# Performance work log

Measured on AMD Instinct MI355X. Metric: run time of the kernel, lower is better.

The kernel has to match this reference:

```python
import jax, jax.numpy as jnp
import numpy as np

GROUPS = 256   # B: number of index groups
SEQ = 512      # L: tokens per group (equal-length groups)
D_IN = 128
D_QK = 64
D_V = 128


def setup_inputs() -> dict:
    key = jax.random.key(0)
    ks = jax.random.split(key, 7)
    N = GROUPS * SEQ
    inputs = jax.random.normal(ks[0], (N, D_IN), dtype=jnp.float32)
    # sorted group ids: GROUPS groups of SEQ tokens each
    index = jnp.repeat(jnp.arange(GROUPS, dtype=jnp.int64), SEQ)
    s_in = 1.0 / np.sqrt(D_IN)
    Wq = jax.random.normal(ks[1], (D_IN, D_QK), dtype=jnp.float32) * s_in
    bq = jax.random.normal(ks[2], (D_QK,), dtype=jnp.float32) * 0.01
    Wk = jax.random.normal(ks[3], (D_IN, D_QK), dtype=jnp.float32) * s_in
    bk = jax.random.normal(ks[4], (D_QK,), dtype=jnp.float32) * 0.01
    Wv = jax.random.normal(ks[5], (D_IN, D_V), dtype=jnp.float32) * s_in
    bv = jax.random.normal(ks[6], (D_V,), dtype=jnp.float32) * 0.01
    return {"inputs": inputs, "index": index, "Wq": Wq, "bq": bq,
            "Wk": Wk, "bk": bk, "Wv": Wv, "bv": bv}


def reference(inputs, index, Wq, bq, Wk, bk, Wv, bv):
    # Linear projections on flat tokens [N, d]
    q = inputs @ Wq + bq          # [N, D_QK]
    k = inputs @ Wk + bk          # [N, D_QK]
    v = inputs @ Wv + bv          # [N, D_V]
    # unbatch: equal-length sorted groups -> [B, L, d]
    q = q.reshape(GROUPS, SEQ, D_QK)
    k = k.reshape(GROUPS, SEQ, D_QK)
    v = v.reshape(GROUPS, SEQ, D_V)
    # note the module's scale: sqrt(2 * d_qk)
    scale = 1.0 / np.sqrt(2.0 * D_QK).astype(np.float32)
    scores = jnp.einsum('bqd,bkd->bqk', q, k) * scale   # [B, L, L]
    attn = jax.nn.softmax(scores, axis=-1)
    out = jnp.einsum('bqk,bkd->bqd', attn, v)           # [B, L, D_V]
    return out.reshape(-1, D_V)                          # [N, D_V]
```

## Files before the change

kernel.cpp:

```cpp
#include <hip/hip_runtime.h>
#include <hip/hip_bf16.h>
#include <stdint.h>

#define GROUPS 256
#define SEQ    512
#define D_IN   128
#define D_QK   64
#define D_V    128
#define NTOK   (GROUPS * SEQ)

#define SL2E (0.08838834764831845f * 1.4426950408889634f)

typedef short bf8 __attribute__((ext_vector_type(8)));
typedef short bf4 __attribute__((ext_vector_type(4)));
typedef float f32x4 __attribute__((ext_vector_type(4)));

__device__ __forceinline__ short f2bf(float f) {
    __bf16 h = (__bf16)f;
    return __builtin_bit_cast(short, h);
}

__device__ __forceinline__ void gload_lds16(const void* g, void* l) {
    __builtin_amdgcn_global_load_lds(
        (const __attribute__((address_space(1))) unsigned int*)(uintptr_t)(g),
        (__attribute__((address_space(3))) unsigned int*)(uint32_t)(uintptr_t)(l),
        16, 0, 0);
}

__global__ __launch_bounds__(256) void prep_w(
    const float* __restrict__ Wq, const float* __restrict__ bq,
    const float* __restrict__ Wk, const float* __restrict__ bk,
    const float* __restrict__ Wv, const float* __restrict__ bv,
    short* __restrict__ Wt, float* __restrict__ bcat)
{
    const int t = blockIdx.x * 256 + threadIdx.x;
    const int r  = t >> 5;
    const int k0 = (t & 31) * 4;
    const float* W; int ld; int c; float sc;
    if (r < 64)       { W = Wq; ld = 64;  c = r;       sc = SL2E; }
    else if (r < 128) { W = Wk; ld = 64;  c = r - 64;  sc = 1.0f; }
    else              { W = Wv; ld = 128; c = r - 128; sc = 1.0f; }
    bf4 pk;
#pragma unroll
    for (int i = 0; i < 4; ++i) pk[i] = f2bf(W[(size_t)(k0 + i) * ld + c] * sc);
    const int phys = (k0 * 2) ^ ((r & 7) << 4);
    *reinterpret_cast<bf4*>((char*)Wt + r * 256 + phys) = pk;
    if (t < 256) {
        const float* b = (t < 64) ? bq : (t < 128 ? bk : bv);
        const int cb   = (t < 64) ? t  : (t < 128 ? t - 64 : t - 128);
        bcat[t] = b[cb] * (t < 64 ? SL2E : 1.0f);
    }
}

__global__ __launch_bounds__(256) void proj_kernel(
    const float* __restrict__ x, const short* __restrict__ Wt,
    const float* __restrict__ bcat,
    short* __restrict__ Q, short* __restrict__ K, short* __restrict__ Vt)
{
    __shared__ short wlds[16384];
    const int tid = threadIdx.x;
    const int wid = tid >> 6, lane = tid & 63, l15 = lane & 15, lg = lane >> 4;

#pragma unroll
    for (int i = 0; i < 8; ++i)
        gload_lds16((const char*)Wt + i * 4096 + tid * 16,
                    (char*)wlds + i * 4096 + tid * 16);

    const size_t tw = (size_t)blockIdx.x * 128 + wid * 32;
    const int g     = (int)(tw >> 9);
    const int tseg  = (int)(tw & 511);

    bf8 xf[2][4];
#pragma unroll
    for (int m = 0; m < 2; ++m) {
        const float* xr = x + (tw + m * 16 + l15) * D_IN;
#pragma unroll
        for (int kf = 0; kf < 4; ++kf) {
            const float4 a = *reinterpret_cast<const float4*>(xr + kf * 32 + lg * 8);
            const float4 b = *reinterpret_cast<const float4*>(xr + kf * 32 + lg * 8 + 4);
            bf8 v;
            v[0] = f2bf(a.x); v[1] = f2bf(a.y); v[2] = f2bf(a.z); v[3] = f2bf(a.w);
            v[4] = f2bf(b.x); v[5] = f2bf(b.y); v[6] = f2bf(b.z); v[7] = f2bf(b.w);
            xf[m][kf] = v;
        }
    }
    __syncthreads();

#pragma unroll
    for (int cf = 0; cf < 8; ++cf) {
        const int wrow = cf * 16 + l15;
        bf8 wf[4];
#pragma unroll
        for (int kf = 0; kf < 4; ++kf) {
            const int off = (kf * 64 + lg * 16) ^ ((wrow & 7) << 4);
            wf[kf] = *reinterpret_cast<const bf8*>((const char*)wlds + wrow * 256 + off);
        }
        const float4 bias4 = *reinterpret_cast<const float4*>(bcat + cf * 16 + lg * 4);
#pragma unroll
        for (int m = 0; m < 2; ++m) {
            f32x4 acc = (f32x4){0.f, 0.f, 0.f, 0.f};
#pragma unroll
            for (int kf = 0; kf < 4; ++kf)
                acc = __builtin_amdgcn_mfma_f32_16x16x32_bf16(wf[kf], xf[m][kf], acc, 0, 0, 0);
            bf4 pk;
            pk[0] = f2bf(acc[0] + bias4.x); pk[1] = f2bf(acc[1] + bias4.y);
            pk[2] = f2bf(acc[2] + bias4.z); pk[3] = f2bf(acc[3] + bias4.w);
            const size_t tok = tw + m * 16 + l15;
            if (cf < 4) {
                *reinterpret_cast<bf4*>((char*)Q + tok * 128 + cf * 32 + lg * 8) = pk;
            } else {
                const int lo = ((cf - 4) * 32 + lg * 8) ^ (((int)tok & 7) << 4);
                *reinterpret_cast<bf4*>((char*)K + tok * 128 + lo) = pk;
            }
        }
    }
    __syncthreads();

#pragma unroll
    for (int i = 0; i < 8; ++i)
        gload_lds16((const char*)Wt + 32768 + i * 4096 + tid * 16,
                    (char*)wlds + i * 4096 + tid * 16);
    __syncthreads();

#pragma unroll
    for (int cf = 8; cf < 16; ++cf) {
        const int lrow = (cf - 8) * 16 + l15;
        bf8 wf[4];
#pragma unroll
        for (int kf = 0; kf < 4; ++kf) {
            const int off = (kf * 64 + lg * 16) ^ ((lrow & 7) << 4);
            wf[kf] = *reinterpret_cast<const bf8*>((const char*)wlds + lrow * 256 + off);
        }
        const int d = (cf - 8) * 16 + l15;
        const float bias = bcat[cf * 16 + l15];
        const int sd = (d >> 1) & 3;
        char* vg = (char*)Vt + (size_t)g * 131072 + (size_t)d * 64;
#pragma unroll
        for (int m = 0; m < 2; ++m) {
            f32x4 acc = (f32x4){0.f, 0.f, 0.f, 0.f};
#pragma unroll
            for (int kf = 0; kf < 4; ++kf)
                acc = __builtin_amdgcn_mfma_f32_16x16x32_bf16(xf[m][kf], wf[kf], acc, 0, 0, 0);
            bf4 pk;
#pragma unroll
            for (int r = 0; r < 4; ++r) pk[r] = f2bf(acc[r] + bias);
            const int t0    = tseg + m * 16;
            const int inner = ((lg ^ sd) << 4) + ((t0 >> 4) & 1) * 8;
            *reinterpret_cast<bf4*>(vg + (size_t)(t0 >> 5) * 8192 + inner) = pk;
        }
    }
}

__global__ __launch_bounds__(256, 4) void attn_kernel(
    const short* __restrict__ Q, const short* __restrict__ K,
    const short* __restrict__ Vt, float* __restrict__ out)
{
    __shared__ short lds[2 * 6144];
    const int g = blockIdx.x, rb = blockIdx.y;
    const int tid = threadIdx.x, wid = tid >> 6, lane = tid & 63;
    const int l15 = lane & 15, lg = lane >> 4;
    const size_t gtok = (size_t)g * SEQ;
    const int row0 = rb * 128 + wid * 32;

    bf8 qf[2][2];
#pragma unroll
    for (int rf = 0; rf < 2; ++rf) {
        const short* qr = Q + (gtok + row0 + rf * 16 + l15) * 64 + lg * 8;
        qf[rf][0] = *reinterpret_cast<const bf8*>(qr);
        qf[rf][1] = *reinterpret_cast<const bf8*>(qr + 32);
    }

    const char* Kg = (const char*)(K + gtok * 64);
    const char* Vg = (const char*)Vt + (size_t)g * 131072;

    f32x4 o[2][8];
#pragma unroll
    for (int rf = 0; rf < 2; ++rf)
#pragma unroll
        for (int vt = 0; vt < 8; ++vt) o[rf][vt] = (f32x4){0.f, 0.f, 0.f, 0.f};
    f32x4 psv[2] = {(f32x4){0.f, 0.f, 0.f, 0.f}, (f32x4){0.f, 0.f, 0.f, 0.f}};
    const bf8 onesf = {0x3F80, 0x3F80, 0x3F80, 0x3F80, 0x3F80, 0x3F80, 0x3F80, 0x3F80};

    auto stage = [&](int kt, int b) {
        char* lbase = (char*)lds + b * 12288;
        int c = wid * 3;
#pragma unroll
        for (int i = 0; i < 3; ++i, ++c) {
            if (c < 4) {
                gload_lds16(Kg + (size_t)kt * 4096 + c * 1024 + lane * 16,
                            lbase + c * 1024 + lane * 16);
            } else {
                gload_lds16(Vg + (size_t)kt * 8192 + (c - 4) * 1024 + lane * 16,
                            lbase + c * 1024 + lane * 16);
            }
        }
    };

    auto compute = [&](int b) {
        const char* lb = (const char*)lds + b * 12288;
        __builtin_amdgcn_s_setprio(1);
        f32x4 st[2][2];
#pragma unroll
        for (int tf = 0; tf < 2; ++tf) {
            const int tok = tf * 16 + l15;
            const char* kb = lb + tok * 128;
            const int x7 = (tok & 7) << 4;
            const bf8 k0 = *reinterpret_cast<const bf8*>(kb + ((lg * 16) ^ x7));
            const bf8 k1 = *reinterpret_cast<const bf8*>(kb + ((64 + lg * 16) ^ x7));
#pragma unroll
            for (int rf = 0; rf < 2; ++rf) {
                f32x4 s = (f32x4){0.f, 0.f, 0.f, 0.f};
                s = __builtin_amdgcn_mfma_f32_16x16x32_bf16(k0, qf[rf][0], s, 0, 0, 0);
                s = __builtin_amdgcn_mfma_f32_16x16x32_bf16(k1, qf[rf][1], s, 0, 0, 0);
                st[tf][rf] = s;
            }
        }
        bf8 pa[2];
#pragma unroll
        for (int rf = 0; rf < 2; ++rf) {
            bf8 pv;
#pragma unroll
            for (int i = 0; i < 4; ++i) {
                pv[i]     = f2bf(__builtin_amdgcn_exp2f(st[0][rf][i]));
                pv[i + 4] = f2bf(__builtin_amdgcn_exp2f(st[1][rf][i]));
            }
            pa[rf] = pv;
            psv[rf] = __builtin_amdgcn_mfma_f32_16x16x32_bf16(pv, onesf, psv[rf], 0, 0, 0);
        }
        const char* vb = lb + 4096;
#pragma unroll
        for (int vt = 0; vt < 8; ++vt) {
            const int d = vt * 16 + l15;
            const char* vr = vb + d * 64;
            const bf8 v0 = *reinterpret_cast<const bf8*>(vr + ((lg * 16) ^ ((((d >> 1) & 3)) << 4)));
            o[0][vt] = __builtin_amdgcn_mfma_f32_16x16x32_bf16(pa[0], v0, o[0][vt], 0, 0, 0);
            o[1][vt] = __builtin_amdgcn_mfma_f32_16x16x32_bf16(pa[1], v0, o[1][vt], 0, 0, 0);
        }
        __builtin_amdgcn_s_setprio(0);
    };

    stage(0, 0);
    __syncthreads();
    for (int kt = 0; kt < 16; ++kt) {
        const int b = kt & 1;
        if (kt < 15) stage(kt + 1, b ^ 1);
        compute(b);
        __syncthreads();
    }

#pragma unroll
    for (int rf = 0; rf < 2; ++rf) {
        float linv[4];
#pragma unroll
        for (int r = 0; r < 4; ++r) linv[r] = 1.0f / psv[rf][r];
        float* op = out + (gtok + row0 + rf * 16) * D_V;
#pragma unroll
        for (int vt = 0; vt < 8; ++vt)
#pragma unroll
            for (int r = 0; r < 4; ++r)
                op[(size_t)(lg * 4 + r) * D_V + vt * 16 + l15] = o[rf][vt][r] * linv[r];
    }
}

extern "C" void kernel_launch(void* const* d_in, const int* in_sizes, int n_in,
                              void* d_out, int out_size, void* d_ws, size_t ws_size,
                              hipStream_t stream) {
    (void)in_sizes; (void)n_in; (void)ws_size; (void)out_size;
    const float* x  = (const float*)d_in[0];
    const float* Wq = (const float*)d_in[2];
    const float* bq = (const float*)d_in[3];
    const float* Wk = (const float*)d_in[4];
    const float* bk = (const float*)d_in[5];
    const float* Wv = (const float*)d_in[6];
    const float* bv = (const float*)d_in[7];
    float* out = (float*)d_out;

    short* Qw = (short*)d_ws;
    short* Kw = Qw + (size_t)NTOK * D_QK;
    short* Vt = Kw + (size_t)NTOK * D_QK;

    short* Wt   = (short*)out;
    float* bcat = (float*)((char*)out + 65536);

    prep_w<<<32, 256, 0, stream>>>(Wq, bq, Wk, bk, Wv, bv, Wt, bcat);
    proj_kernel<<<NTOK / 128, 256, 0, stream>>>(x, Wt, bcat, Qw, Kw, Vt);
    attn_kernel<<<dim3(GROUPS, 4), 256, 0, stream>>>(Qw, Kw, Vt, out);
}
```

Baseline: 67.96 us.

## Fuse QKV projection into attention kernel, one block per group

Merges the projection and attention kernels into one kernel that runs one 512-thread block per group. Q is projected once into registers, and K/V are recomputed per 32-token tile from x staged in LDS. This removes the Q/K/Vt workspace round-trip through global memory and one launch. In exchange, the grid drops from 1024 blocks to 256 blocks, each using about 108KB of LDS and many registers, which lowers occupancy and parallelism. Every K/V projection step now sits on the critical path, separated from the attention math by an added barrier.

```diff
diff --git a/kernel.cpp b/kernel.cpp
--- a/kernel.cpp
+++ b/kernel.cpp
@@ -5,8 +5,6 @@
 #define GROUPS 256
 #define SEQ    512
 #define D_IN   128
-#define D_QK   64
-#define D_V    128
 #define NTOK   (GROUPS * SEQ)
 
 #define SL2E (0.08838834764831845f * 1.4426950408889634f)
@@ -52,28 +50,27 @@
     }
 }
 
-__global__ __launch_bounds__(256) void proj_kernel(
+__global__ __launch_bounds__(512, 2) void fused_kernel(
     const float* __restrict__ x, const short* __restrict__ Wt,
-    const float* __restrict__ bcat,
-    short* __restrict__ Q, short* __restrict__ K, short* __restrict__ Vt)
+    const float* __restrict__ bcat, float* __restrict__ out)
 {
-    __shared__ short wlds[16384];
+    extern __shared__ char smem[];
     const int tid = threadIdx.x;
-    const int wid = tid >> 6, lane = tid & 63, l15 = lane & 15, lg = lane >> 4;
+    const int w = tid >> 6, lane = tid & 63, l15 = lane & 15, lg = lane >> 4;
+    const int g = blockIdx.x;
+    char* Wl  = smem;
+    char* xb0 = smem + 65536;
+    char* xb1 = smem + 81920;
+    char* kv  = smem + 98304;
 
 #pragma unroll
     for (int i = 0; i < 8; ++i)
-        gload_lds16((const char*)Wt + i * 4096 + tid * 16,
-                    (char*)wlds + i * 4096 + tid * 16);
-
-    const size_t tw = (size_t)blockIdx.x * 128 + wid * 32;
-    const int g     = (int)(tw >> 9);
-    const int tseg  = (int)(tw & 511);
-
-    bf8 xf[2][4];
-#pragma unroll
-    for (int m = 0; m < 2; ++m) {
-        const float* xr = x + (tw + m * 16 + l15) * D_IN;
+        gload_lds16((const char*)Wt + i * 8192 + tid * 16, Wl + i * 8192 + tid * 16);
+
+    bf8 xq[4][4];
+#pragma unroll
+    for (int rf = 0; rf < 4; ++rf) {
+        const float* xr = x + ((size_t)g * SEQ + w * 64 + rf * 16 + l15) * D_IN;
 #pragma unroll
         for (int kf = 0; kf < 4; ++kf) {
             const float4 a = *reinterpret_cast<const float4*>(xr + kf * 32 + lg * 8);
@@ -81,143 +78,159 @@
             bf8 v;
             v[0] = f2bf(a.x); v[1] = f2bf(a.y); v[2] = f2bf(a.z); v[3] = f2bf(a.w);
             v[4] = f2bf(b.x); v[5] = f2bf(b.y); v[6] = f2bf(b.z); v[7] = f2bf(b.w);
-            xf[m][kf] = v;
-        }
-    }
+            xq[rf][kf] = v;
+        }
+    }
+
+    int ucf[3], utb[3], uIsK[3];
+    float4 ub4[3]; float ubS[3];
+#pragma unroll
+    for (int ui = 0; ui < 3; ++ui) {
+        const int u = w * 3 + ui;
+        if (u < 8) {
+            uIsK[ui] = 1; ucf[ui] = u >> 1; utb[ui] = u & 1;
+            ub4[ui] = *reinterpret_cast<const float4*>(bcat + (4 + ucf[ui]) * 16 + lg * 4);
+            ubS[ui] = 0.f;
+        } else {
+            const int v = u - 8;
+            uIsK[ui] = 0; ucf[ui] = v >> 1; utb[ui] = v & 1;
+            ubS[ui] = bcat[(8 + ucf[ui]) * 16 + l15];
+            ub4[ui] = (float4){0.f, 0.f, 0.f, 0.f};
+        }
+    }
+
     __syncthreads();
 
-#pragma unroll
-    for (int cf = 0; cf < 8; ++cf) {
-        const int wrow = cf * 16 + l15;
-        bf8 wf[4];
-#pragma unroll
-        for (int kf = 0; kf < 4; ++kf) {
-            const int off = (kf * 64 + lg * 16) ^ ((wrow & 7) << 4);
-            wf[kf] = *reinterpret_cast<const bf8*>((const char*)wlds + wrow * 256 + off);
-        }
-        const float4 bias4 = *reinterpret_cast<const float4*>(bcat + cf * 16 + lg * 4);
-#pragma unroll
-        for (int m = 0; m < 2; ++m) {
+    bf8 qf[4][2];
+    char* qs = xb0 + w * 4096;
+#pragma unroll
+    for (int rf = 0; rf < 4; ++rf) {
+        char* q2 = qs + (rf & 1) * 2048;
+#pragma unroll
+        for (int cf = 0; cf < 4; ++cf) {
+            const int wrow = cf * 16 + l15;
+            bf8 wf[4];
+#pragma unroll
+            for (int kf = 0; kf < 4; ++kf) {
+                const int off = (kf * 64 + lg * 16) ^ ((wrow & 7) << 4);
+                wf[kf] = *reinterpret_cast<const bf8*>(Wl + wrow * 256 + off);
+            }
+            const float4 b4 = *reinterpret_cast<const float4*>(bcat + cf * 16 + lg * 4);
             f32x4 acc = (f32x4){0.f, 0.f, 0.f, 0.f};
 #pragma unroll
             for (int kf = 0; kf < 4; ++kf)
-                acc = __builtin_amdgcn_mfma_f32_16x16x32_bf16(wf[kf], xf[m][kf], acc, 0, 0, 0);
+                acc = __builtin_amdgcn_mfma_f32_16x16x32_bf16(wf[kf], xq[rf][kf], acc, 0, 0, 0);
             bf4 pk;
-            pk[0] = f2bf(acc[0] + bias4.x); pk[1] = f2bf(acc[1] + bias4.y);
-            pk[2] = f2bf(acc[2] + bias4.z); pk[3] = f2bf(acc[3] + bias4.w);
-            const size_t tok = tw + m * 16 + l15;
-            if (cf < 4) {
-                *reinterpret_cast<bf4*>((char*)Q + tok * 128 + cf * 32 + lg * 8) = pk;
+            pk[0] = f2bf(acc[0] + b4.x); pk[1] = f2bf(acc[1] + b4.y);
+            pk[2] = f2bf(acc[2] + b4.z); pk[3] = f2bf(acc[3] + b4.w);
+            *reinterpret_cast<bf4*>(q2 + (cf * 2 + (lg >> 1)) * 256 + l15 * 16 + (lg & 1) * 8) = pk;
+        }
+        qf[rf][0] = *reinterpret_cast<const bf8*>(q2 + lg * 256 + l15 * 16);
+        qf[rf][1] = *reinterpret_cast<const bf8*>(q2 + (4 + lg) * 256 + l15 * 16);
+    }
+    __syncthreads();
+
+    const char* xg = (const char*)x + (size_t)g * SEQ * 512;
+    auto stageX = [&](int kt, char* dst) {
+        const char* xsrc = xg + (size_t)kt * 32 * 512;
+#pragma unroll
+        for (int i = 0; i < 2; ++i) {
+            const int cph  = i * 512 + tid;
+            const int tok  = cph >> 5;
+            const int lchk = (cph & 31) ^ (tok & 7);
+            gload_lds16(xsrc + (size_t)tok * 512 + lchk * 16, dst + cph * 16);
+        }
+    };
+
+    stageX(0, xb0);
+    __syncthreads();
+
+    f32x4 o[4][8];
+#pragma unroll
+    for (int rf = 0; rf < 4; ++rf)
+#pragma unroll
+        for (int vt = 0; vt < 8; ++vt) o[rf][vt] = (f32x4){0.f, 0.f, 0.f, 0.f};
+    f32x4 psv[4] = {(f32x4){0.f,0.f,0.f,0.f}, (f32x4){0.f,0.f,0.f,0.f},
+                    (f32x4){0.f,0.f,0.f,0.f}, (f32x4){0.f,0.f,0.f,0.f}};
+    const bf8 onesf = {0x3F80, 0x3F80, 0x3F80, 0x3F80, 0x3F80, 0x3F80, 0x3F80, 0x3F80};
+
+#pragma unroll 1
+    for (int kt = 0; kt < 16; ++kt) {
+        if (kt < 15) stageX(kt + 1, (kt & 1) ? xb0 : xb1);
+
+        const char* xbc = (kt & 1) ? xb1 : xb0;
+#pragma unroll
+        for (int ui = 0; ui < 3; ++ui) {
+            const int cf = ucf[ui], tb = utb[ui];
+            const int xrow = tb * 16 + l15;
+            const int sx = xrow & 7;
+            bf8 xf[4];
+#pragma unroll
+            for (int kf = 0; kf < 4; ++kf) {
+                const int c0 = (kf * 8 + lg * 2)     ^ sx;
+                const int c1 = (kf * 8 + lg * 2 + 1) ^ sx;
+                const f32x4 a = *reinterpret_cast<const f32x4*>(xbc + xrow * 512 + c0 * 16);
+                const f32x4 b = *reinterpret_cast<const f32x4*>(xbc + xrow * 512 + c1 * 16);
+                bf8 v;
+                v[0] = f2bf(a[0]); v[1] = f2bf(a[1]); v[2] = f2bf(a[2]); v[3] = f2bf(a[3]);
+                v[4] = f2bf(b[0]); v[5] = f2bf(b[1]); v[6] = f2bf(b[2]); v[7] = f2bf(b[3]);
+                xf[kf] = v;
+            }
+            if (uIsK[ui]) {
+                const int wrow = 64 + cf * 16 + l15;
+                bf8 wf[4];
+#pragma unroll
+                for (int kf = 0; kf < 4; ++kf) {
+                    const int off = (kf * 64 + lg * 16) ^ ((wrow & 7) << 4);
+                    wf[kf] = *reinterpret_cast<const bf8*>(Wl + wrow * 256 + off);
+                }
+                f32x4 acc = (f32x4){0.f, 0.f, 0.f, 0.f};
+#pragma unroll
+                for (int kf = 0; kf < 4; ++kf)
+                    acc = __builtin_amdgcn_mfma_f32_16x16x32_bf16(wf[kf], xf[kf], acc, 0, 0, 0);
+                bf4 pk;
+                pk[0] = f2bf(acc[0] + ub4[ui].x); pk[1] = f2bf(acc[1] + ub4[ui].y);
+                pk[2] = f2bf(acc[2] + ub4[ui].z); pk[3] = f2bf(acc[3] + ub4[ui].w);
+                *reinterpret_cast<bf4*>(kv + (cf * 2 + (lg >> 1)) * 512 + xrow * 16 + (lg & 1) * 8) = pk;
             } else {
-                const int lo = ((cf - 4) * 32 + lg * 8) ^ (((int)tok & 7) << 4);
-                *reinterpret_cast<bf4*>((char*)K + tok * 128 + lo) = pk;
-            }
-        }
-    }
-    __syncthreads();
-
-#pragma unroll
-    for (int i = 0; i < 8; ++i)
-        gload_lds16((const char*)Wt + 32768 + i * 4096 + tid * 16,
-                    (char*)wlds + i * 4096 + tid * 16);
-    __syncthreads();
-
-#pragma unroll
-    for (int cf = 8; cf < 16; ++cf) {
-        const int lrow = (cf - 8) * 16 + l15;
-        bf8 wf[4];
-#pragma unroll
-        for (int kf = 0; kf < 4; ++kf) {
-            const int off = (kf * 64 + lg * 16) ^ ((lrow & 7) << 4);
-            wf[kf] = *reinterpret_cast<const bf8*>((const char*)wlds + lrow * 256 + off);
-        }
-        const int d = (cf - 8) * 16 + l15;
-        const float bias = bcat[cf * 16 + l15];
-        const int sd = (d >> 1) & 3;
-        char* vg = (char*)Vt + (size_t)g * 131072 + (size_t)d * 64;
-#pragma unroll
-        for (int m = 0; m < 2; ++m) {
-            f32x4 acc = (f32x4){0.f, 0.f, 0.f, 0.f};
-#pragma unroll
-            for (int kf = 0; kf < 4; ++kf)
-                acc = __builtin_amdgcn_mfma_f32_16x16x32_bf16(xf[m][kf], wf[kf], acc, 0, 0, 0);
-            bf4 pk;
-#pragma unroll
-            for (int r = 0; r < 4; ++r) pk[r] = f2bf(acc[r] + bias);
-            const int t0    = tseg + m * 16;
-            const int inner = ((lg ^ sd) << 4) + ((t0 >> 4) & 1) * 8;
-            *reinterpret_cast<bf4*>(vg + (size_t)(t0 >> 5) * 8192 + inner) = pk;
-        }
-    }
-}
-
-__global__ __launch_bounds__(256, 4) void attn_kernel(
-    const short* __restrict__ Q, const short* __restrict__ K,
-    const short* __restrict__ Vt, float* __restrict__ out)
-{
-    __shared__ short lds[2 * 6144];
-    const int g = blockIdx.x, rb = blockIdx.y;
-    const int tid = threadIdx.x, wid = tid >> 6, lane = tid & 63;
-    const int l15 = lane & 15, lg = lane >> 4;
-    const size_t gtok = (size_t)g * SEQ;
-    const int row0 = rb * 128 + wid * 32;
-
-    bf8 qf[2][2];
-#pragma unroll
-    for (int rf = 0; rf < 2; ++rf) {
-        const short* qr = Q + (gtok + row0 + rf * 16 + l15) * 64 + lg * 8;
-        qf[rf][0] = *reinterpret_cast<const bf8*>(qr);
-        qf[rf][1] = *reinterpret_cast<const bf8*>(qr + 32);
-    }
-
-    const char* Kg = (const char*)(K + gtok * 64);
-    const char* Vg = (const char*)Vt + (size_t)g * 131072;
-
-    f32x4 o[2][8];
-#pragma unroll
-    for (int rf = 0; rf < 2; ++rf)
-#pragma unroll
-        for (int vt = 0; vt < 8; ++vt) o[rf][vt] = (f32x4){0.f, 0.f, 0.f, 0.f};
-    f32x4 psv[2] = {(f32x4){0.f, 0.f, 0.f, 0.f}, (f32x4){0.f, 0.f, 0.f, 0.f}};
-    const bf8 onesf = {0x3F80, 0x3F80, 0x3F80, 0x3F80, 0x3F80, 0x3F80, 0x3F80, 0x3F80};
-
-    auto stage = [&](int kt, int b) {
-        char* lbase = (char*)lds + b * 12288;
-        int c = wid * 3;
-#pragma unroll
-        for (int i = 0; i < 3; ++i, ++c) {
-            if (c < 4) {
-                gload_lds16(Kg + (size_t)kt * 4096 + c * 1024 + lane * 16,
-                            lbase + c * 1024 + lane * 16);
-            } else {
-                gload_lds16(Vg + (size_t)kt * 8192 + (c - 4) * 1024 + lane * 16,
-                            lbase + c * 1024 + lane * 16);
-            }
-        }
-    };
-
-    auto compute = [&](int b) {
-        const char* lb = (const char*)lds + b * 12288;
+                const int wrow = 128 + cf * 16 + l15;
+                bf8 wf[4];
+#pragma unroll
+                for (int kf = 0; kf < 4; ++kf) {
+                    const int off = (kf * 64 + lg * 16) ^ ((wrow & 7) << 4);
+                    wf[kf] = *reinterpret_cast<const bf8*>(Wl + wrow * 256 + off);
+                }
+                f32x4 acc = (f32x4){0.f, 0.f, 0.f, 0.f};
+#pragma unroll
+                for (int kf = 0; kf < 4; ++kf)
+                    acc = __builtin_amdgcn_mfma_f32_16x16x32_bf16(xf[kf], wf[kf], acc, 0, 0, 0);
+                const int d = cf * 16 + l15;
+                bf4 pk;
+#pragma unroll
+                for (int r = 0; r < 4; ++r) pk[r] = f2bf(acc[r] + ubS[ui]);
+                *reinterpret_cast<bf4*>(kv + 4096 + lg * 2048 + d * 16 + tb * 8) = pk;
+            }
+        }
+        __syncthreads();
+
         __builtin_amdgcn_s_setprio(1);
-        f32x4 st[2][2];
+        f32x4 st[2][4];
 #pragma unroll
         for (int tf = 0; tf < 2; ++tf) {
             const int tok = tf * 16 + l15;
-            const char* kb = lb + tok * 128;
-            const int x7 = (tok & 7) << 4;
-            const bf8 k0 = *reinterpret_cast<const bf8*>(kb + ((lg * 16) ^ x7));
-            const bf8 k1 = *reinterpret_cast<const bf8*>(kb + ((64 + lg * 16) ^ x7));
-#pragma unroll
-            for (int rf = 0; rf < 2; ++rf) {
+            const bf8 k0 = *reinterpret_cast<const bf8*>(kv + lg * 512       + tok * 16);
+            const bf8 k1 = *reinterpret_cast<const bf8*>(kv + (4 + lg) * 512 + tok * 16);
+#pragma unroll
+            for (int rf = 0; rf < 4; ++rf) {
                 f32x4 s = (f32x4){0.f, 0.f, 0.f, 0.f};
                 s = __builtin_amdgcn_mfma_f32_16x16x32_bf16(k0, qf[rf][0], s, 0, 0, 0);
                 s = __builtin_amdgcn_mfma_f32_16x16x32_bf16(k1, qf[rf][1], s, 0, 0, 0);
                 st[tf][rf] = s;
             }
         }
-        bf8 pa[2];
-#pragma unroll
-        for (int rf = 0; rf < 2; ++rf) {
+        bf8 pa[4];
+#pragma unroll
+        for (int rf = 0; rf < 4; ++rf) {
             bf8 pv;
 #pragma unroll
             for (int i = 0; i < 4; ++i) {
@@ -227,38 +240,29 @@
             pa[rf] = pv;
             psv[rf] = __builtin_amdgcn_mfma_f32_16x16x32_bf16(pv, onesf, psv[rf], 0, 0, 0);
         }
-        const char* vb = lb + 4096;
 #pragma unroll
         for (int vt = 0; vt < 8; ++vt) {
             const int d = vt * 16 + l15;
-            const char* vr = vb + d * 64;
-            const bf8 v0 = *reinterpret_cast<const bf8*>(vr + ((lg * 16) ^ ((((d >> 1) & 3)) << 4)));
-            o[0][vt] = __builtin_amdgcn_mfma_f32_16x16x32_bf16(pa[0], v0, o[0][vt], 0, 0, 0);
-            o[1][vt] = __builtin_amdgcn_mfma_f32_16x16x32_bf16(pa[1], v0, o[1][vt], 0, 0, 0);
+            const bf8 v0 = *reinterpret_cast<const bf8*>(kv + 4096 + lg * 2048 + d * 16);
+#pragma unroll
+            for (int rf = 0; rf < 4; ++rf)
+                o[rf][vt] = __builtin_amdgcn_mfma_f32_16x16x32_bf16(pa[rf], v0, o[rf][vt], 0, 0, 0);
         }
         __builtin_amdgcn_s_setprio(0);
-    };
-
-    stage(0, 0);
-    __syncthreads();
-    for (int kt = 0; kt < 16; ++kt) {
-        const int b = kt & 1;
-        if (kt < 15) stage(kt + 1, b ^ 1);
-        compute(b);
         __syncthreads();
     }
 
 #pragma unroll
-    for (int rf = 0; rf < 2; ++rf) {
+    for (int rf = 0; rf < 4; ++rf) {
         float linv[4];
 #pragma unroll
         for (int r = 0; r < 4; ++r) linv[r] = 1.0f / psv[rf][r];
-        float* op = out + (gtok + row0 + rf * 16) * D_V;
+        float* op = out + ((size_t)g * SEQ + w * 64 + rf * 16) * 128;
 #pragma unroll
         for (int vt = 0; vt < 8; ++vt)
 #pragma unroll
             for (int r = 0; r < 4; ++r)
-                op[(size_t)(lg * 4 + r) * D_V + vt * 16 + l15] = o[rf][vt][r] * linv[r];
+                op[(size_t)(lg * 4 + r) * 128 + vt * 16 + l15] = o[rf][vt][r] * linv[r];
     }
 }
 
@@ -275,14 +279,12 @@
     const float* bv = (const float*)d_in[7];
     float* out = (float*)d_out;
 
-    short* Qw = (short*)d_ws;
-    short* Kw = Qw + (size_t)NTOK * D_QK;
-    short* Vt = Kw + (size_t)NTOK * D_QK;
-
-    short* Wt   = (short*)out;
-    float* bcat = (float*)((char*)out + 65536);
+    short* Wt   = (short*)d_ws;
+    float* bcat = (float*)((char*)d_ws + 65536);
+
+    hipFuncSetAttribute((const void*)fused_kernel,
+                        hipFuncAttributeMaxDynamicSharedMemorySize, 110592);
 
     prep_w<<<32, 256, 0, stream>>>(Wq, bq, Wk, bk, Wv, bv, Wt, bcat);
-    proj_kernel<<<NTOK / 128, 256, 0, stream>>>(x, Wt, bcat, Qw, Kw, Vt);
-    attn_kernel<<<dim3(GROUPS, 4), 256, 0, stream>>>(Qw, Kw, Vt, out);
-}
+    fused_kernel<<<GROUPS, 512, 110592, stream>>>(x, Wt, bcat, out);
+}
```

New measurement: 83.96 us. +23.5%, slower.
